# Kernel tuning notes

Measured on AMD Instinct MI355X. Metric: run time of the kernel, lower is better.

Reference implementation:

```python
import jax, jax.numpy as jnp
import numpy as np

B, CI, CO, H, W = 16, 32, 32, 256, 256
K0, K1 = 32, 32              # modes_fourier
LEVEL0, LEVEL1 = 3, 5        # PDEPara_mode_level
M = 2 ** LEVEL1              # 32 = modes_pde_extra per dim
KAPPA = (2 * M) // (2 ** LEVEL0)  # 8 = kappa_base
NPARA = 3 * (LEVEL0 - 1) + 1      # 7 columns of fourierweight_scaling used


def setup_inputs() -> dict:
    key = jax.random.key(0)
    ks = jax.random.split(key, 6)
    scale = 1.0 / (CI * CO)
    x = jax.random.normal(ks[0], (B, CI, H, W), dtype=jnp.float32)
    fourierweight_scaling = jax.random.uniform(ks[1], (B, NPARA), dtype=jnp.float32)
    weights_dim0 = scale * jax.random.uniform(ks[2], (CI, CO, K0, K1, 2), dtype=jnp.float32)
    weights_dim1 = scale * jax.random.uniform(ks[3], (CI, CO, K0, K1, 2), dtype=jnp.float32)
    weights_extra_dim0 = scale * jax.random.uniform(ks[4], (CI, CO, M, M, 2), dtype=jnp.float32)
    weights_extra_dim1 = scale * jax.random.uniform(ks[5], (CI, CO, M, M, 2), dtype=jnp.float32)
    return dict(x=x, fourierweight_scaling=fourierweight_scaling,
                weights_dim0=weights_dim0, weights_dim1=weights_dim1,
                weights_extra_dim0=weights_extra_dim0, weights_extra_dim1=weights_extra_dim1)


def _c(w):
    # real-pair [..., 2] -> complex; compl2/compl3_einsum are exactly complex products
    return jax.lax.complex(w[..., 0], w[..., 1])


def _mode_scaling(fs):
    # hierarchical quadrant-wise per-mode scaling, [B, M, M]
    s = jnp.zeros((B, M, M), dtype=fs.dtype)
    s = s.at[:, :KAPPA, :KAPPA].set(fs[:, 0][:, None, None])
    for d in range(1, LEVEL0):  # small fixed number of levels
        l0 = KAPPA * 2 ** (d - 1)
        l1 = 2 * l0
        s = s.at[:, :l0, l0:l1].set(fs[:, 3 * d - 2][:, None, None])
        s = s.at[:, l0:l1, :l0].set(fs[:, 3 * d - 1][:, None, None])
        s = s.at[:, l0:l1, l0:l1].set(fs[:, 3 * d][:, None, None])
    return s


def reference(x, fourierweight_scaling, weights_dim0, weights_dim1,
              weights_extra_dim0, weights_extra_dim1):
    x_ft = jnp.fft.rfft2(x, norm='ortho')  # [B, CI, H, W//2+1] complex
    out_ft = jnp.zeros((B, CO, H, W // 2 + 1), dtype=x_ft.dtype)
    # base mode mixing on low / high row-frequency corners
    out_ft = out_ft.at[:, :, :K0, :K1].set(
        jnp.einsum('bixy,ioxy->boxy', x_ft[:, :, :K0, :K1], _c(weights_dim0)))
    out_ft = out_ft.at[:, :, -K0:, :K1].set(
        jnp.einsum('bixy,ioxy->boxy', x_ft[:, :, -K0:, :K1], _c(weights_dim1)))
    # PDE-parameter dependent extra mixing with hierarchical scaling
    s = _mode_scaling(fourierweight_scaling).astype(x_ft.dtype)
    out_ft = out_ft.at[:, :, :M, :M].add(
        jnp.einsum('bixy,ioxy,bxy->boxy', x_ft[:, :, :M, :M], _c(weights_extra_dim0), s))
    out_ft = out_ft.at[:, :, -M:, :M].add(
        jnp.einsum('bixy,ioxy,bxy->boxy', x_ft[:, :, -M:, :M], _c(weights_extra_dim1), s))
    return jnp.fft.irfft2(out_ft, s=(H, W), norm='ortho')  # [B, CO, H, W]
```

## Files before the change

### kernel.cpp

```cpp
#include <hip/hip_runtime.h>


typedef _Float16 f16;
typedef _Float16 f16x8 __attribute__((ext_vector_type(8)));
typedef float f32x4 __attribute__((ext_vector_type(4)));

__global__ void k_tabs(f16* __restrict__ Etab, f16* __restrict__ Ftabt,
                       f16* __restrict__ Etab2, f16* __restrict__ Tt) {
    const int h = blockIdx.x;
    const int tid = threadIdx.x;
    if (tid < 64) {
        const int j = tid;
        const int ky = (j < 32) ? j : j - 64;
        float s, c;
        sincospif((float)(ky * h) / 128.0f, &s, &c);
        Etab[h * 128 + 2 * j] = (f16)c;
        Etab[h * 128 + 2 * j + 1] = (f16)s;
        Etab2[j * 512 + 2 * h] = (f16)c;
        Etab2[j * 512 + 2 * h + 1] = (f16)s;
    } else if (tid < 96) {
        const int k = tid - 64;
        const float ck = (k == 0) ? 1.0f : 2.0f;
        float s, c;
        sincospif((float)(k * h) / 128.0f, &s, &c);
        Ftabt[h * 64 + 2 * k] = (f16)(ck * c);
        Ftabt[h * 64 + 2 * k + 1] = (f16)(-ck * s);
    } else {
        const int kx = tid - 96;
        float s, c;
        sincospif((float)(kx * h) / 128.0f, &s, &c);
        Tt[(2 * kx) * 256 + h] = (f16)c;
        Tt[(2 * kx + 1) * 256 + h] = (f16)(-s);
    }
}

__global__ __launch_bounds__(256) void k_rowdftB(const float* __restrict__ x,
                                                 const f16* __restrict__ Tt,
                                                 f16* __restrict__ Xw16) {
    __shared__ __align__(16) f16 Gs[128 * 88];
    const int tid = threadIdx.x;
    const int wv = tid >> 6, lane = tid & 63;
    const int l15 = lane & 15, lk = lane >> 4;
    const long rowbase = (long)blockIdx.x * 128;

    f32x4 acc[2][4];
#pragma unroll
    for (int mt = 0; mt < 2; ++mt)
#pragma unroll
        for (int nt = 0; nt < 4; ++nt)
            acc[mt][nt] = (f32x4){0.0f, 0.0f, 0.0f, 0.0f};

    const float* xbase = x + (rowbase + wv * 32 + l15) * 256 + lk * 8;
    const f16* tbase = Tt + l15 * 256 + lk * 8;

#pragma unroll
    for (int ks = 0; ks < 8; ++ks) {
        f16x8 a[2], b[4];
#pragma unroll
        for (int mt = 0; mt < 2; ++mt) {
            const float4 u = *(const float4*)(xbase + mt * 4096 + ks * 32);
            const float4 v = *(const float4*)(xbase + mt * 4096 + ks * 32 + 4);
            a[mt][0] = (f16)u.x; a[mt][1] = (f16)u.y;
            a[mt][2] = (f16)u.z; a[mt][3] = (f16)u.w;
            a[mt][4] = (f16)v.x; a[mt][5] = (f16)v.y;
            a[mt][6] = (f16)v.z; a[mt][7] = (f16)v.w;
        }
#pragma unroll
        for (int nt = 0; nt < 4; ++nt)
            b[nt] = *(const f16x8*)(tbase + nt * 4096 + ks * 32);
#pragma unroll
        for (int mt = 0; mt < 2; ++mt)
#pragma unroll
            for (int nt = 0; nt < 4; ++nt)
                acc[mt][nt] = __builtin_amdgcn_mfma_f32_16x16x32_f16(
                    a[mt], b[nt], acc[mt][nt], 0, 0, 0);
    }

#pragma unroll
    for (int mt = 0; mt < 2; ++mt)
#pragma unroll
        for (int nt = 0; nt < 4; ++nt) {
            const int row0 = wv * 32 + mt * 16 + lk * 4;
            const int col = nt * 16 + l15;
#pragma unroll
            for (int r = 0; r < 4; ++r)
                Gs[(row0 + r) * 88 + col] = (f16)acc[mt][nt][r];
        }
    __syncthreads();

#pragma unroll
    for (int p = 0; p < 4; ++p) {
        const int id = p * 256 + tid;
        const int row = id >> 3, ch = id & 7;
        *(uint4*)(Xw16 + (rowbase + row) * 64 + ch * 8) =
            *(const uint4*)(Gs + row * 88 + ch * 8);
    }
}

__global__ __launch_bounds__(256) void k_coldftB(const f16* __restrict__ Xw16,
                                                 const f16* __restrict__ Etab2,
                                                 float* __restrict__ Xf) {
    __shared__ __align__(16) f16 Bt[64 * 520];
    const int tid = threadIdx.x;
    const long p = blockIdx.x;

    {
        const uint* src = (const uint*)(Xw16 + (p * 256 + tid) * 64);
        uint* B32 = (uint*)Bt;
#pragma unroll
        for (int kx = 0; kx < 32; ++kx) {
            const uint a = src[kx];
            const uint b = (a >> 16) | (((a & 0xffffu) ^ 0x8000u) << 16);
            B32[(2 * kx) * 260 + tid] = a;
            B32[(2 * kx + 1) * 260 + tid] = b;
        }
    }
    __syncthreads();

    const int wv = tid >> 6, lane = tid & 63;
    const int l15 = lane & 15, lk = lane >> 4;

    f32x4 acc[4];
#pragma unroll
    for (int nt = 0; nt < 4; ++nt) acc[nt] = (f32x4){0.0f, 0.0f, 0.0f, 0.0f};

    const f16* abase = Etab2 + (wv * 16 + l15) * 512 + lk * 8;
#pragma unroll
    for (int ks = 0; ks < 16; ++ks) {
        const f16x8 a = *(const f16x8*)(abase + ks * 32);
        f16x8 b[4];
#pragma unroll
        for (int nt = 0; nt < 4; ++nt)
            b[nt] = *(const f16x8*)(Bt + (nt * 16 + l15) * 520 + ks * 32 + lk * 8);
#pragma unroll
        for (int nt = 0; nt < 4; ++nt)
            acc[nt] = __builtin_amdgcn_mfma_f32_16x16x32_f16(a, b[nt], acc[nt], 0, 0, 0);
    }

    float* obase = Xf + p * 4096;
#pragma unroll
    for (int nt = 0; nt < 4; ++nt)
#pragma unroll
        for (int r = 0; r < 4; ++r)
            obase[(wv * 16 + lk * 4 + r) * 64 + nt * 16 + l15] = acc[nt][r];
}

__global__ __launch_bounds__(256) void k_mix(const float* __restrict__ Xf,
                                             const float* __restrict__ fs,
                                             const float* __restrict__ w0,
                                             const float* __restrict__ w1,
                                             const float* __restrict__ we0,
                                             const float* __restrict__ we1,
                                             float* __restrict__ Ff) {
    __shared__ float2 xv[512];
    __shared__ float2 wsw[1024];
    __shared__ float2 wse[1024];
    __shared__ float sv[16];
    const int tid = threadIdx.x;
    const int j = blockIdx.x >> 5, kx = blockIdx.x & 31;
    const int jj = j & 31;
    const float* W = (j < 32) ? w0 : w1;
    const float* We = (j < 32) ? we0 : we1;
    const int moff = (jj * 32 + kx) * 2;
    const int foff = (j * 32 + kx) * 2;

    for (int t = tid; t < 512; t += 256)
        xv[t] = *(const float2*)(Xf + (long)t * 4096 + foff);
    for (int t = tid; t < 1024; t += 256) {
        wsw[t] = *(const float2*)(W + (long)t * 2048 + moff);
        wse[t] = *(const float2*)(We + (long)t * 2048 + moff);
    }
    if (tid < 16) {
        const int u = jj, v = kx;
        int idx;
        if (u < 8 && v < 8) idx = 0;
        else if (u < 16 && v < 16) idx = (u < 8) ? 1 : ((v < 8) ? 2 : 3);
        else idx = (u < 16) ? 4 : ((v < 16) ? 5 : 6);
        sv[tid] = fs[tid * 7 + idx];
    }
    __syncthreads();

    for (int t = tid; t < 512; t += 256) {
        const int b = t >> 5, co = t & 31;
        const float s = sv[b];
        float re = 0.0f, im = 0.0f;
#pragma unroll 8
        for (int ci = 0; ci < 32; ++ci) {
            const float2 xc = xv[b * 32 + ci];
            const float2 wc = wsw[ci * 32 + co];
            const float2 ec = wse[ci * 32 + co];
            const float mr = wc.x + s * ec.x;
            const float mi = wc.y + s * ec.y;
            re += xc.x * mr - xc.y * mi;
            im += xc.x * mi + xc.y * mr;
        }
        *(float2*)(Ff + (long)t * 4096 + foff) = make_float2(re, im);
    }
}

__global__ __launch_bounds__(256) void k_invB(const float* __restrict__ Ff,
                                              const f16* __restrict__ Etab,
                                              f16* __restrict__ Gbuf) {
    __shared__ __align__(16) f16 Ft[64 * 136];
    __shared__ __align__(16) f16 Gs[256 * 72];
    const int tid = threadIdx.x;
    const long q = blockIdx.x;

    {
        const float4* src = (const float4*)(Ff + q * 4096);
        float4 v[4];
#pragma unroll
        for (int i = 0; i < 4; ++i) v[i] = src[tid * 4 + i];
#pragma unroll
        for (int i = 0; i < 4; ++i) {
            const float* f = &v[i].x;
#pragma unroll
            for (int p = 0; p < 4; p += 2) {
                const int idx = tid * 16 + i * 4 + p;
                const int j = idx >> 6, kx = (idx >> 1) & 31;
                const float fr = f[p], fi = f[p + 1];
                Ft[(2 * kx) * 136 + 2 * j] = (f16)fr;
                Ft[(2 * kx) * 136 + 2 * j + 1] = (f16)(-fi);
                Ft[(2 * kx + 1) * 136 + 2 * j] = (f16)fi;
                Ft[(2 * kx + 1) * 136 + 2 * j + 1] = (f16)fr;
            }
        }
    }
    __syncthreads();

    const int wv = tid >> 6, lane = tid & 63;
    const int l15 = lane & 15, lk = lane >> 4;

    f32x4 acc[4][4];
#pragma unroll
    for (int mt = 0; mt < 4; ++mt)
#pragma unroll
        for (int nt = 0; nt < 4; ++nt)
            acc[mt][nt] = (f32x4){0.0f, 0.0f, 0.0f, 0.0f};

    const f16* Arow = Etab + (wv * 64 + l15) * 128 + lk * 8;
#pragma unroll
    for (int ks = 0; ks < 4; ++ks) {
        f16x8 a[4], b[4];
#pragma unroll
        for (int mt = 0; mt < 4; ++mt)
            a[mt] = *(const f16x8*)(Arow + mt * 2048 + ks * 32);
#pragma unroll
        for (int nt = 0; nt < 4; ++nt)
            b[nt] = *(const f16x8*)(&Ft[(nt * 16 + l15) * 136 + ks * 32 + lk * 8]);
#pragma unroll
        for (int mt = 0; mt < 4; ++mt)
#pragma unroll
            for (int nt = 0; nt < 4; ++nt)
                acc[mt][nt] = __builtin_amdgcn_mfma_f32_16x16x32_f16(
                    a[mt], b[nt], acc[mt][nt], 0, 0, 0);
    }

#pragma unroll
    for (int mt = 0; mt < 4; ++mt)
#pragma unroll
        for (int nt = 0; nt < 4; ++nt) {
            const int row = wv * 64 + mt * 16 + lk * 4;
            const int col = nt * 16 + l15;
#pragma unroll
            for (int r = 0; r < 4; ++r)
                Gs[(row + r) * 72 + col] = (f16)acc[mt][nt][r];
        }
    __syncthreads();

#pragma unroll
    for (int p = 0; p < 8; ++p) {
        const int id = p * 256 + tid;
        const int row = id >> 3, ch = id & 7;
        const uint4 u = *(const uint4*)(Gs + row * 72 + ch * 8);
        *(uint4*)(Gbuf + q * 16384 + row * 64 + ch * 8) = u;
    }
}

__global__ __launch_bounds__(256) void k_invC(const f16* __restrict__ Gbuf,
                                              const f16* __restrict__ Ftabt,
                                              float* __restrict__ out) {
    const int tid = threadIdx.x;
    const long q = blockIdx.x >> 1;
    const int half = blockIdx.x & 1;
    const int wv = tid >> 6, lane = tid & 63;
    const int l15 = lane & 15, lk = lane >> 4;

    f16x8 a[2][2];
    const f16* abase = Gbuf + q * 16384 + (half * 128 + wv * 32 + l15) * 64 + lk * 8;
#pragma unroll
    for (int mt = 0; mt < 2; ++mt)
#pragma unroll
        for (int ks = 0; ks < 2; ++ks)
            a[mt][ks] = *(const f16x8*)(abase + mt * 1024 + ks * 32);

    float* obase = out + q * 65536 + (long)(half * 128 + wv * 32) * 256;

#pragma unroll 1
    for (int g = 0; g < 4; ++g) {
        f32x4 acc[2][4];
#pragma unroll
        for (int mt = 0; mt < 2; ++mt)
#pragma unroll
            for (int nt = 0; nt < 4; ++nt)
                acc[mt][nt] = (f32x4){0.0f, 0.0f, 0.0f, 0.0f};

        const f16* bbase = Ftabt + (g * 64 + l15) * 64 + lk * 8;
#pragma unroll
        for (int nt = 0; nt < 4; ++nt)
#pragma unroll
            for (int ks = 0; ks < 2; ++ks) {
                const f16x8 b = *(const f16x8*)(bbase + nt * 1024 + ks * 32);
#pragma unroll
                for (int mt = 0; mt < 2; ++mt)
                    acc[mt][nt] = __builtin_amdgcn_mfma_f32_16x16x32_f16(
                        a[mt][ks], b, acc[mt][nt], 0, 0, 0);
            }

#pragma unroll
        for (int mt = 0; mt < 2; ++mt)
#pragma unroll
            for (int nt = 0; nt < 4; ++nt) {
                float* o = obase + (mt * 16 + lk * 4) * 256 + g * 64 + nt * 16 + l15;
#pragma unroll
                for (int r = 0; r < 4; ++r)
                    o[r * 256] = acc[mt][nt][r] * 0x1p-16f;
            }
    }
}

extern "C" void kernel_launch(void* const* d_in, const int* in_sizes, int n_in,
                              void* d_out, int out_size, void* d_ws, size_t ws_size,
                              hipStream_t stream) {
    (void)in_sizes; (void)n_in; (void)out_size; (void)ws_size;
    const float* x   = (const float*)d_in[0];
    const float* fs  = (const float*)d_in[1];
    const float* w0  = (const float*)d_in[2];
    const float* w1  = (const float*)d_in[3];
    const float* we0 = (const float*)d_in[4];
    const float* we1 = (const float*)d_in[5];
    float* out = (float*)d_out;
    float* ws = (float*)d_ws;

    f16* Etab   = (f16*)ws;
    f16* Ftabt  = (f16*)(ws + 16384);
    f16* Etab2  = (f16*)(ws + 24576);
    f16* Tt     = (f16*)(ws + 40960);
    f16* Xw16   = (f16*)(ws + 49152);
    f16* Gbuf   = (f16*)(ws + 49152 + 4194304);
    float* Xf   = ws + 49152 + 8388608;
    float* Ff   = Xf + 2097152;

    k_tabs   <<<256,  128, 0, stream>>>(Etab, Ftabt, Etab2, Tt);
    k_rowdftB<<<1024, 256, 0, stream>>>(x, Tt, Xw16);
    k_coldftB<<<512,  256, 0, stream>>>(Xw16, Etab2, Xf);
    k_mix    <<<2048, 256, 0, stream>>>(Xf, fs, w0, w1, we0, we1, Ff);
    k_invB   <<<512,  256, 0, stream>>>(Ff, Etab, Gbuf);
    k_invC   <<<1024, 256, 0, stream>>>(Gbuf, Ftabt, out);
}
```

Baseline: 360.9 us.

## Store spectral intermediates in fp16 and restructure mode-mixing kernel for weight reuse

The column-DFT output and the mixed spectrum are now stored as packed fp16 complex values instead of fp32, which halves the intermediate traffic. The mixing kernel is rewritten so that each block stages a slab of base and extra weights in swizzled shared memory and gives each thread two kx modes and four output channels. The base and extra products are accumulated separately and combined with the per-batch scale at the end. The inverse kernel's staging is simplified to bit-level sign flips and half swaps on the packed fp16 data, at the cost of reduced precision in the intermediates.

```diff
diff --git a/kernel.cpp b/kernel.cpp
--- a/kernel.cpp
+++ b/kernel.cpp
@@ -4,6 +4,15 @@
 typedef _Float16 f16;
 typedef _Float16 f16x8 __attribute__((ext_vector_type(8)));
 typedef float f32x4 __attribute__((ext_vector_type(4)));
+
+static __device__ __forceinline__ float2 upk(uint u) {
+    union { uint x; f16 h[2]; } c; c.x = u;
+    return make_float2((float)c.h[0], (float)c.h[1]);
+}
+static __device__ __forceinline__ uint pk2(float r, float i) {
+    union { uint x; f16 h[2]; } c; c.h[0] = (f16)r; c.h[1] = (f16)i;
+    return c.x;
+}
 
 __global__ void k_tabs(f16* __restrict__ Etab, f16* __restrict__ Ftabt,
                        f16* __restrict__ Etab2, f16* __restrict__ Tt) {
@@ -99,7 +108,7 @@
 
 __global__ __launch_bounds__(256) void k_coldftB(const f16* __restrict__ Xw16,
                                                  const f16* __restrict__ Etab2,
-                                                 float* __restrict__ Xf) {
+                                                 f16* __restrict__ Xf16) {
     __shared__ __align__(16) f16 Bt[64 * 520];
     const int tid = threadIdx.x;
     const long p = blockIdx.x;
@@ -137,68 +146,90 @@
             acc[nt] = __builtin_amdgcn_mfma_f32_16x16x32_f16(a, b[nt], acc[nt], 0, 0, 0);
     }
 
-    float* obase = Xf + p * 4096;
+    f16* obase = Xf16 + p * 4096;
 #pragma unroll
     for (int nt = 0; nt < 4; ++nt)
 #pragma unroll
         for (int r = 0; r < 4; ++r)
-            obase[(wv * 16 + lk * 4 + r) * 64 + nt * 16 + l15] = acc[nt][r];
-}
-
-__global__ __launch_bounds__(256) void k_mix(const float* __restrict__ Xf,
-                                             const float* __restrict__ fs,
-                                             const float* __restrict__ w0,
-                                             const float* __restrict__ w1,
-                                             const float* __restrict__ we0,
-                                             const float* __restrict__ we1,
-                                             float* __restrict__ Ff) {
-    __shared__ float2 xv[512];
-    __shared__ float2 wsw[1024];
-    __shared__ float2 wse[1024];
-    __shared__ float sv[16];
-    const int tid = threadIdx.x;
-    const int j = blockIdx.x >> 5, kx = blockIdx.x & 31;
-    const int jj = j & 31;
-    const float* W = (j < 32) ? w0 : w1;
-    const float* We = (j < 32) ? we0 : we1;
-    const int moff = (jj * 32 + kx) * 2;
-    const int foff = (j * 32 + kx) * 2;
-
-    for (int t = tid; t < 512; t += 256)
-        xv[t] = *(const float2*)(Xf + (long)t * 4096 + foff);
-    for (int t = tid; t < 1024; t += 256) {
-        wsw[t] = *(const float2*)(W + (long)t * 2048 + moff);
-        wse[t] = *(const float2*)(We + (long)t * 2048 + moff);
-    }
-    if (tid < 16) {
-        const int u = jj, v = kx;
+            obase[(wv * 16 + lk * 4 + r) * 64 + nt * 16 + l15] = (f16)acc[nt][r];
+}
+
+__global__ __launch_bounds__(256) void k_mixB(const f16* __restrict__ Xf16,
+                                              const float* __restrict__ fs,
+                                              const float* __restrict__ w0,
+                                              const float* __restrict__ w1,
+                                              const float* __restrict__ we0,
+                                              const float* __restrict__ we1,
+                                              f16* __restrict__ Ff16) {
+    __shared__ __align__(16) float4 Wl[4096];
+    const int tid = threadIdx.x;
+    const int bid = blockIdx.x;
+    const int cog = bid >> 6;
+    const int corner = (bid >> 5) & 1;
+    const int jj = bid & 31;
+    const int j = corner * 32 + jj;
+
+    {
+        const int t = tid >> 7, ci = (tid >> 2) & 31, co = tid & 3;
+        const float* Wt = (t == 0) ? (corner ? w1 : w0) : (corner ? we1 : we0);
+        const float4* src =
+            (const float4*)(Wt + ((long)(ci * 32 + cog * 4 + co) * 2048 + jj * 64));
+        const int m = tid & 15;
+#pragma unroll
+        for (int i = 0; i < 16; ++i) Wl[tid * 16 + (i ^ m)] = src[i];
+    }
+    __syncthreads();
+
+    const int b = tid >> 4, kxp = tid & 15;
+    const int kx0 = 2 * kxp;
+
+    float s[2];
+#pragma unroll
+    for (int e = 0; e < 2; ++e) {
+        const int v = kx0 + e, u = jj;
         int idx;
         if (u < 8 && v < 8) idx = 0;
         else if (u < 16 && v < 16) idx = (u < 8) ? 1 : ((v < 8) ? 2 : 3);
         else idx = (u < 16) ? 4 : ((v < 16) ? 5 : 6);
-        sv[tid] = fs[tid * 7 + idx];
-    }
-    __syncthreads();
-
-    for (int t = tid; t < 512; t += 256) {
-        const int b = t >> 5, co = t & 31;
-        const float s = sv[b];
-        float re = 0.0f, im = 0.0f;
-#pragma unroll 8
-        for (int ci = 0; ci < 32; ++ci) {
-            const float2 xc = xv[b * 32 + ci];
-            const float2 wc = wsw[ci * 32 + co];
-            const float2 ec = wse[ci * 32 + co];
-            const float mr = wc.x + s * ec.x;
-            const float mi = wc.y + s * ec.y;
-            re += xc.x * mr - xc.y * mi;
-            im += xc.x * mi + xc.y * mr;
-        }
-        *(float2*)(Ff + (long)t * 4096 + foff) = make_float2(re, im);
-    }
-}
-
-__global__ __launch_bounds__(256) void k_invB(const float* __restrict__ Ff,
+        s[e] = fs[b * 7 + idx];
+    }
+
+    float aW[4][4] = {}, aE[4][4] = {};
+    const uint* xb = (const uint*)Xf16 + (long)(b * 32) * 2048 + j * 32 + kx0;
+
+    for (int ci = 0; ci < 32; ++ci) {
+        const uint2 xu = *(const uint2*)(xb + ci * 2048);
+        const float2 x0 = upk(xu.x), x1 = upk(xu.y);
+        const int rbase = ci * 4;
+#pragma unroll
+        for (int co = 0; co < 4; ++co) {
+            const int rw = rbase + co;
+            const int sl = kxp ^ (rw & 15);
+            const float4 wv = Wl[rw * 16 + sl];
+            const float4 ev = Wl[(128 + rw) * 16 + sl];
+            aW[co][0] += x0.x * wv.x - x0.y * wv.y;
+            aW[co][1] += x0.x * wv.y + x0.y * wv.x;
+            aW[co][2] += x1.x * wv.z - x1.y * wv.w;
+            aW[co][3] += x1.x * wv.w + x1.y * wv.z;
+            aE[co][0] += x0.x * ev.x - x0.y * ev.y;
+            aE[co][1] += x0.x * ev.y + x0.y * ev.x;
+            aE[co][2] += x1.x * ev.z - x1.y * ev.w;
+            aE[co][3] += x1.x * ev.w + x1.y * ev.z;
+        }
+    }
+
+    uint* ofb = (uint*)Ff16;
+#pragma unroll
+    for (int co = 0; co < 4; ++co) {
+        const long q = b * 32 + cog * 4 + co;
+        uint2 o;
+        o.x = pk2(aW[co][0] + s[0] * aE[co][0], aW[co][1] + s[0] * aE[co][1]);
+        o.y = pk2(aW[co][2] + s[1] * aE[co][2], aW[co][3] + s[1] * aE[co][3]);
+        *(uint2*)(ofb + q * 2048 + j * 32 + kx0) = o;
+    }
+}
+
+__global__ __launch_bounds__(256) void k_invB(const f16* __restrict__ Ff16,
                                               const f16* __restrict__ Etab,
                                               f16* __restrict__ Gbuf) {
     __shared__ __align__(16) f16 Ft[64 * 136];
@@ -207,22 +238,19 @@
     const long q = blockIdx.x;
 
     {
-        const float4* src = (const float4*)(Ff + q * 4096);
-        float4 v[4];
-#pragma unroll
-        for (int i = 0; i < 4; ++i) v[i] = src[tid * 4 + i];
-#pragma unroll
-        for (int i = 0; i < 4; ++i) {
-            const float* f = &v[i].x;
-#pragma unroll
-            for (int p = 0; p < 4; p += 2) {
-                const int idx = tid * 16 + i * 4 + p;
-                const int j = idx >> 6, kx = (idx >> 1) & 31;
-                const float fr = f[p], fi = f[p + 1];
-                Ft[(2 * kx) * 136 + 2 * j] = (f16)fr;
-                Ft[(2 * kx) * 136 + 2 * j + 1] = (f16)(-fi);
-                Ft[(2 * kx + 1) * 136 + 2 * j] = (f16)fi;
-                Ft[(2 * kx + 1) * 136 + 2 * j + 1] = (f16)fr;
+        const uint4* src = (const uint4*)(Ff16 + q * 4096);
+        uint* B32 = (uint*)Ft;
+#pragma unroll
+        for (int i = 0; i < 2; ++i) {
+            const uint4 v = src[tid * 2 + i];
+            const uint a4[4] = {v.x, v.y, v.z, v.w};
+#pragma unroll
+            for (int c = 0; c < 4; ++c) {
+                const int idx = tid * 8 + i * 4 + c;
+                const int jr = idx >> 5, kx = idx & 31;
+                const uint a = a4[c];
+                B32[(2 * kx) * 68 + jr] = a ^ 0x80000000u;
+                B32[(2 * kx + 1) * 68 + jr] = (a >> 16) | (a << 16);
             }
         }
     }
@@ -348,13 +376,13 @@
     f16* Tt     = (f16*)(ws + 40960);
     f16* Xw16   = (f16*)(ws + 49152);
     f16* Gbuf   = (f16*)(ws + 49152 + 4194304);
-    float* Xf   = ws + 49152 + 8388608;
-    float* Ff   = Xf + 2097152;
+    f16* Xf16   = (f16*)(ws + 49152 + 8388608);
+    f16* Ff16   = (f16*)(ws + 49152 + 8388608 + 2097152);
 
     k_tabs   <<<256,  128, 0, stream>>>(Etab, Ftabt, Etab2, Tt);
     k_rowdftB<<<1024, 256, 0, stream>>>(x, Tt, Xw16);
-    k_coldftB<<<512,  256, 0, stream>>>(Xw16, Etab2, Xf);
-    k_mix    <<<2048, 256, 0, stream>>>(Xf, fs, w0, w1, we0, we1, Ff);
-    k_invB   <<<512,  256, 0, stream>>>(Ff, Etab, Gbuf);
+    k_coldftB<<<512,  256, 0, stream>>>(Xw16, Etab2, Xf16);
+    k_mixB   <<<512,  256, 0, stream>>>(Xf16, fs, w0, w1, we0, we1, Ff16);
+    k_invB   <<<512,  256, 0, stream>>>(Ff16, Etab, Gbuf);
     k_invC   <<<1024, 256, 0, stream>>>(Gbuf, Ftabt, out);
 }
```

Result: faster. 319.7 us (-11.4%).
